# Performance work log

Measured on AMD Instinct MI355X. Metric: run time of the kernel, lower is better.

## Reference

```python
import jax, jax.numpy as jnp
import numpy as np

B, S, E, H = 8, 2048, 512, 4
D = E // H


def setup_inputs() -> dict:
    key = jax.random.key(0)
    ks = jax.random.split(key, 9)
    std = 0.05  # keras 'normal' initializer default stddev
    return {
        "x": jax.random.normal(ks[0], (B, S, E), dtype=jnp.float32),
        "Wq": jax.random.normal(ks[1], (E, E), dtype=jnp.float32) * std,
        "Wk": jax.random.normal(ks[2], (E, E), dtype=jnp.float32) * std,
        "Wv": jax.random.normal(ks[3], (E, E), dtype=jnp.float32) * std,
        "Wepi": jax.random.normal(ks[4], (S, S), dtype=jnp.float32) * std,
        "bq": jax.random.normal(ks[5], (S, 1), dtype=jnp.float32) * std,
        "bk": jax.random.normal(ks[6], (S, 1), dtype=jnp.float32) * std,
        "bv": jax.random.normal(ks[7], (S, 1), dtype=jnp.float32) * std,
        "bo": jax.random.normal(ks[8], (S, 1), dtype=jnp.float32) * std,
    }


def reference(x, Wq, Wk, Wv, Wepi, bq, bk, bv, bo):
    b, s, e = x.shape
    # QKV projections; [S,1] biases broadcast across the feature dim
    q = x @ Wq + bq  # [B,S,E]
    k = x @ Wk + bk
    v = x @ Wv + bv
    # split heads -> [B,H,S,D]
    q = q.reshape(b, s, H, D).transpose(0, 2, 1, 3)
    k = k.reshape(b, s, H, D).transpose(0, 2, 1, 3)
    v = v.reshape(b, s, H, D).transpose(0, 2, 1, 3)
    # NOTE: source scales by sqrt(seq_length), not sqrt(head_dim)
    scale = 1.0 / np.sqrt(float(s)).astype(np.float32)
    scores = jnp.einsum("bhsd,bhtd->bhst", q, k) * scale  # [B,H,S,S]
    attn = jax.nn.softmax(scores, axis=-1)
    # epigenomic multiplicative mask applied AFTER softmax (broadcast [S,S])
    attn = attn * Wepi
    effect = jnp.einsum("bhst,bhtd->bhsd", attn, v)  # [B,H,S,D]
    effect = effect.transpose(0, 2, 1, 3).reshape(b, s, e) + bo
    # original returns attention in merged-batch layout [B*H, S, S]
    return effect, attn.reshape(b * H, s, s)
```

## Files before the change

### kernel.cpp

```cpp
#include <hip/hip_runtime.h>
#include <hip/hip_bf16.h>

constexpr int Bn = 8, Sn = 2048, En = 512, Hn = 4, Dn = 128;
constexpr int BHn = Bn * Hn;
constexpr int Mqkv = Bn * Sn;

typedef __attribute__((ext_vector_type(8))) short short8;
typedef __attribute__((ext_vector_type(4))) float f32x4;

__device__ __forceinline__ unsigned short f2bf(float f) {
  unsigned int u = __builtin_bit_cast(unsigned int, f);
  u += 0x7FFF + ((u >> 16) & 1);
  return (unsigned short)(u >> 16);
}

__device__ __forceinline__ void bar_pub() {
  asm volatile("s_waitcnt lgkmcnt(0)" ::: "memory");
  __builtin_amdgcn_s_barrier();
  asm volatile("" ::: "memory");
}

__global__ __launch_bounds__(256) void qkv_kernel(
    const float* __restrict__ x, const float* __restrict__ Wq,
    const float* __restrict__ Wk, const float* __restrict__ Wv,
    const float* __restrict__ bq, const float* __restrict__ bk,
    const float* __restrict__ bv, unsigned short* __restrict__ qkv) {
  const int z = blockIdx.z;
  const float* W = (z == 0) ? Wq : (z == 1 ? Wk : Wv);
  const float* bias = (z == 0) ? bq : (z == 1 ? bk : bv);
  unsigned short* out = qkv + (size_t)z * BHn * Sn * Dn;

  __shared__ unsigned short As[128][40];
  __shared__ unsigned short BsT[128][40];

  const int t = threadIdx.x;
  const int l = t & 63, w = t >> 6;
  const int wm = w >> 1, wn = w & 1;
  const int m0 = blockIdx.x * 128, n0 = blockIdx.y * 128;

  f32x4 acc[4][4] = {};

  for (int k0 = 0; k0 < En; k0 += 32) {
    __syncthreads();
#pragma unroll
    for (int i = 0; i < 4; ++i) {
      int idx = t + i * 256;
      int row = idx >> 3, c4 = (idx & 7) * 4;
      float4 v = *reinterpret_cast<const float4*>(&x[(size_t)(m0 + row) * En + k0 + c4]);
      ushort4 p;
      p.x = f2bf(v.x); p.y = f2bf(v.y); p.z = f2bf(v.z); p.w = f2bf(v.w);
      *reinterpret_cast<ushort4*>(&As[row][c4]) = p;
    }
#pragma unroll
    for (int i = 0; i < 4; ++i) {
      int idx = t + i * 256;
      int kk = idx >> 5, c4 = (idx & 31) * 4;
      float4 v = *reinterpret_cast<const float4*>(&W[(size_t)(k0 + kk) * En + n0 + c4]);
      BsT[c4 + 0][kk] = f2bf(v.x);
      BsT[c4 + 1][kk] = f2bf(v.y);
      BsT[c4 + 2][kk] = f2bf(v.z);
      BsT[c4 + 3][kk] = f2bf(v.w);
    }
    __syncthreads();

    const int koff = (l >> 4) * 8;
    short8 a[4], bfr[4];
#pragma unroll
    for (int m = 0; m < 4; ++m)
      a[m] = *reinterpret_cast<const short8*>(&As[wm * 64 + m * 16 + (l & 15)][koff]);
#pragma unroll
    for (int n = 0; n < 4; ++n)
      bfr[n] = *reinterpret_cast<const short8*>(&BsT[wn * 64 + n * 16 + (l & 15)][koff]);
#pragma unroll
    for (int m = 0; m < 4; ++m)
#pragma unroll
      for (int n = 0; n < 4; ++n)
        acc[m][n] = __builtin_amdgcn_mfma_f32_16x16x32_bf16(a[m], bfr[n], acc[m][n], 0, 0, 0);
  }

#pragma unroll
  for (int m = 0; m < 4; ++m)
#pragma unroll
    for (int n = 0; n < 4; ++n)
#pragma unroll
      for (int j = 0; j < 4; ++j) {
        int row = m0 + wm * 64 + m * 16 + (l >> 4) * 4 + j;
        int col = n0 + wn * 64 + n * 16 + (l & 15);
        int s = row & (Sn - 1);
        float v = acc[m][n][j] + bias[s];
        int b = row >> 11;
        int h = col >> 7, d = col & 127;
        out[(size_t)((b * Hn + h) * Sn + s) * Dn + d] = f2bf(v);
      }
}

__global__ __launch_bounds__(256) void vtrans_kernel(
    const unsigned short* __restrict__ v, unsigned short* __restrict__ vT) {
  const int s0 = blockIdx.x * 64, d0 = blockIdx.y * 64;
  const int bh = blockIdx.z;
  const unsigned short* vp = v + (size_t)bh * Sn * Dn;
  unsigned short* op = vT + (size_t)bh * Dn * Sn;
  __shared__ unsigned short Ls[64][72];
  const int t = threadIdx.x;
#pragma unroll
  for (int it = 0; it < 2; ++it) {
    int flat = t + it * 256;
    int r = flat >> 3, cc = flat & 7;
    *reinterpret_cast<short8*>(&Ls[r][cc * 8]) =
        *reinterpret_cast<const short8*>(&vp[(size_t)(s0 + r) * Dn + d0 + cc * 8]);
  }
  __syncthreads();
#pragma unroll
  for (int it = 0; it < 2; ++it) {
    int flat = t + it * 256;
    int d = flat >> 3, sc = flat & 7;
    short8 o;
#pragma unroll
    for (int jo = 0; jo < 8; ++jo) {
      int jj = (jo + sc) & 7;
      o[jj] = (short)Ls[sc * 8 + jj][d];
    }
    *reinterpret_cast<short8*>(&op[(size_t)(d0 + d) * Sn + s0 + sc * 8]) = o;
  }
}

__global__ __launch_bounds__(256, 2) void fused_attn4_kernel(
    const unsigned short* __restrict__ qkv, const unsigned short* __restrict__ vT,
    const float* __restrict__ Wepi, const float* __restrict__ bo,
    float* __restrict__ attn, float* __restrict__ effect) {
  const int bh = blockIdx.y;
  const int s0 = blockIdx.x * 64;
  const unsigned short* qp = qkv + (size_t)bh * Sn * Dn;
  const unsigned short* kp = qkv + (size_t)(BHn + bh) * Sn * Dn;
  const unsigned short* vt = vT + (size_t)bh * Dn * Sn;

  __shared__ unsigned short Kb[2][64 * 128];
  __shared__ unsigned short Vt[2][128 * 64];
  __shared__ unsigned short Psw[4][16 * 72];

  const int t = threadIdx.x, l = t & 63, w = t >> 6;
  const int g = l >> 4, i = l & 15;
  const float scale = 0.022097086912079608f;

  short8 aq[4];
#pragma unroll
  for (int ks = 0; ks < 4; ++ks)
    aq[ks] = *reinterpret_cast<const short8*>(
        &qp[(size_t)(s0 + w * 16 + i) * Dn + ks * 32 + g * 8]);

  int ksrc[4], kdst[4], vsrc[4], vdst[4];
#pragma unroll
  for (int it = 0; it < 4; ++it) {
    int flat = t + it * 256;
    int r = flat >> 4, cc = flat & 15;
    ksrc[it] = r * Dn + cc * 8;
    kdst[it] = r * 128 + ((cc ^ (r & 15)) << 3);
    int d = flat >> 3, ct = flat & 7;
    vsrc[it] = d * Sn + ct * 8;
    vdst[it] = d * 64 + ((ct ^ (d & 7)) << 3);
  }

  short8 kreg[4];
#pragma unroll
  for (int it = 0; it < 4; ++it)
    kreg[it] = *reinterpret_cast<const short8*>(&kp[ksrc[it]]);
#pragma unroll
  for (int it = 0; it < 4; ++it)
    *reinterpret_cast<short8*>(&Kb[0][kdst[it]]) = kreg[it];
#pragma unroll
  for (int it = 0; it < 4; ++it)
    kreg[it] = *reinterpret_cast<const short8*>(&kp[(size_t)64 * Dn + ksrc[it]]);
  bar_pub();

  float rs = 0.f;
  for (int kt = 0; kt < 32; ++kt) {
    const int b = kt & 1;
    f32x4 accT[4] = {};
    __builtin_amdgcn_s_setprio(1);
#pragma unroll
    for (int ks = 0; ks < 4; ++ks)
#pragma unroll
      for (int tf = 0; tf < 4; ++tf) {
        short8 ak = *reinterpret_cast<const short8*>(
            &Kb[b][(tf * 16 + i) * 128 + (((ks * 4 + g) ^ i) << 3)]);
        accT[tf] = __builtin_amdgcn_mfma_f32_16x16x32_bf16(ak, aq[ks], accT[tf], 0, 0, 0);
      }
    __builtin_amdgcn_s_setprio(0);
    float p0 = 0.f, p1 = 0.f;
#pragma unroll
    for (int tf = 0; tf < 4; ++tf) {
      p0 += __expf(accT[tf][0] * scale) + __expf(accT[tf][1] * scale);
      p1 += __expf(accT[tf][2] * scale) + __expf(accT[tf][3] * scale);
    }
    rs += p0 + p1;
    if (kt < 31) {
#pragma unroll
      for (int it = 0; it < 4; ++it)
        *reinterpret_cast<short8*>(&Kb[b ^ 1][kdst[it]]) = kreg[it];
      if (kt < 30)
#pragma unroll
        for (int it = 0; it < 4; ++it)
          kreg[it] = *reinterpret_cast<const short8*>(
              &kp[(size_t)(kt + 2) * 64 * Dn + ksrc[it]]);
    }
    bar_pub();
  }
  rs += __shfl_xor(rs, 16);
  rs += __shfl_xor(rs, 32);
  const float rinv = 1.0f / rs;

  short8 vreg[4];
#pragma unroll
  for (int it = 0; it < 4; ++it) {
    kreg[it] = *reinterpret_cast<const short8*>(&kp[ksrc[it]]);
    vreg[it] = *reinterpret_cast<const short8*>(&vt[vsrc[it]]);
  }
#pragma unroll
  for (int it = 0; it < 4; ++it) {
    *reinterpret_cast<short8*>(&Kb[0][kdst[it]]) = kreg[it];
    *reinterpret_cast<short8*>(&Vt[0][vdst[it]]) = vreg[it];
  }
#pragma unroll
  for (int it = 0; it < 4; ++it) {
    kreg[it] = *reinterpret_cast<const short8*>(&kp[(size_t)64 * Dn + ksrc[it]]);
    vreg[it] = *reinterpret_cast<const short8*>(&vt[64 + vsrc[it]]);
  }
  const float* wrow = Wepi + (size_t)(s0 + w * 16 + i) * Sn + g * 4;
  float4 wr[4];
#pragma unroll
  for (int tf = 0; tf < 4; ++tf)
    wr[tf] = *reinterpret_cast<const float4*>(&wrow[tf * 16]);
  bar_pub();

  f32x4 pv[8] = {};
  float* arow = attn + (size_t)bh * Sn * Sn + (size_t)(s0 + w * 16 + i) * Sn;

  for (int kt = 0; kt < 32; ++kt) {
    const int b = kt & 1;
    const int t0 = kt * 64;
    f32x4 accT[4] = {};
    __builtin_amdgcn_s_setprio(1);
#pragma unroll
    for (int ks = 0; ks < 4; ++ks)
#pragma unroll
      for (int tf = 0; tf < 4; ++tf) {
        short8 ak = *reinterpret_cast<const short8*>(
            &Kb[b][(tf * 16 + i) * 128 + (((ks * 4 + g) ^ i) << 3)]);
        accT[tf] = __builtin_amdgcn_mfma_f32_16x16x32_bf16(ak, aq[ks], accT[tf], 0, 0, 0);
      }
    __builtin_amdgcn_s_setprio(0);

    float4 nwr[4];
    if (kt < 31)
#pragma unroll
      for (int tf = 0; tf < 4; ++tf)
        nwr[tf] = *reinterpret_cast<const float4*>(&wrow[t0 + 64 + tf * 16]);

#pragma unroll
    for (int tf = 0; tf < 4; ++tf) {
      float q0 = __expf(accT[tf][0] * scale) * rinv * wr[tf].x;
      float q1 = __expf(accT[tf][1] * scale) * rinv * wr[tf].y;
      float q2 = __expf(accT[tf][2] * scale) * rinv * wr[tf].z;
      float q3 = __expf(accT[tf][3] * scale) * rinv * wr[tf].w;
      float4 pf4 = {q0, q1, q2, q3};
      *reinterpret_cast<float4*>(&arow[t0 + tf * 16 + g * 4]) = pf4;
      ushort4 pk;
      pk.x = f2bf(q0); pk.y = f2bf(q1); pk.z = f2bf(q2); pk.w = f2bf(q3);
      *reinterpret_cast<ushort4*>(&Psw[w][i * 72 + tf * 16 + g * 4]) = pk;
    }

    __builtin_amdgcn_s_setprio(1);
#pragma unroll
    for (int ks2 = 0; ks2 < 2; ++ks2) {
      short8 pa = *reinterpret_cast<const short8*>(&Psw[w][i * 72 + ks2 * 32 + g * 8]);
#pragma unroll
      for (int df = 0; df < 8; ++df) {
        const int d = df * 16 + i;
        short8 bv = *reinterpret_cast<const short8*>(
            &Vt[b][d * 64 + (((ks2 * 4 + g) ^ (d & 7)) << 3)]);
        pv[df] = __builtin_amdgcn_mfma_f32_16x16x32_bf16(pa, bv, pv[df], 0, 0, 0);
      }
    }
    __builtin_amdgcn_s_setprio(0);

    if (kt < 31) {
#pragma unroll
      for (int it = 0; it < 4; ++it) {
        *reinterpret_cast<short8*>(&Kb[b ^ 1][kdst[it]]) = kreg[it];
        *reinterpret_cast<short8*>(&Vt[b ^ 1][vdst[it]]) = vreg[it];
      }
      if (kt < 30)
#pragma unroll
        for (int it = 0; it < 4; ++it) {
          kreg[it] = *reinterpret_cast<const short8*>(
              &kp[(size_t)(t0 + 128) * Dn + ksrc[it]]);
          vreg[it] = *reinterpret_cast<const short8*>(&vt[t0 + 128 + vsrc[it]]);
        }
#pragma unroll
      for (int tf = 0; tf < 4; ++tf) wr[tf] = nwr[tf];
    }
    bar_pub();
  }

  const int b_ = bh >> 2, h_ = bh & 3;
#pragma unroll
  for (int j = 0; j < 4; ++j) {
    const int row = s0 + w * 16 + g * 4 + j;
    const float bias = bo[row];
#pragma unroll
    for (int df = 0; df < 8; ++df)
      effect[(size_t)(b_ * Sn + row) * En + h_ * Dn + df * 16 + i] = pv[df][j] + bias;
  }
}

extern "C" void kernel_launch(void* const* d_in, const int* in_sizes, int n_in,
                              void* d_out, int out_size, void* d_ws, size_t ws_size,
                              hipStream_t stream) {
  const float* x    = (const float*)d_in[0];
  const float* Wq   = (const float*)d_in[1];
  const float* Wk   = (const float*)d_in[2];
  const float* Wv   = (const float*)d_in[3];
  const float* Wepi = (const float*)d_in[4];
  const float* bq   = (const float*)d_in[5];
  const float* bk   = (const float*)d_in[6];
  const float* bv   = (const float*)d_in[7];
  const float* bo   = (const float*)d_in[8];

  float* effect = (float*)d_out;
  float* attn = effect + (size_t)Bn * Sn * En;
  unsigned short* qkv = (unsigned short*)d_ws;
  unsigned short* vT = qkv + (size_t)3 * BHn * Sn * Dn;

  qkv_kernel<<<dim3(Mqkv / 128, En / 128, 3), 256, 0, stream>>>(x, Wq, Wk, Wv, bq, bk, bv, qkv);
  vtrans_kernel<<<dim3(Sn / 64, Dn / 64, BHn), 256, 0, stream>>>(
      qkv + (size_t)2 * BHn * Sn * Dn, vT);
  fused_attn4_kernel<<<dim3(Sn / 64, BHn), 256, 0, stream>>>(qkv, vT, Wepi, bo, attn, effect);
}
```

Baseline: 411.1 us.

## Repartition attention warps over key columns and head-dim, software-pipeline PV by one tile

Each wave now holds all 64 query rows in registers and computes scores for its own 16-key slice, so every K fragment loaded from LDS is reused across four MFMAs instead of one. The PV product is split across waves by head-dim slice, with P shared through a double-buffered, swizzled LDS tile and its MFMAs delayed by one iteration so they overlap the next tile's QK^T. Row sums for the softmax are reduced across waves through LDS. This cuts LDS traffic for K and V fragments, but it raises register pressure (16 Q fragments held per wave) and adds a cross-wave reduction plus extra LDS for P.

```diff
diff --git a/kernel.cpp b/kernel.cpp
--- a/kernel.cpp
+++ b/kernel.cpp
@@ -124,7 +124,7 @@
   }
 }
 
-__global__ __launch_bounds__(256, 2) void fused_attn4_kernel(
+__global__ __launch_bounds__(256, 2) void fused_attn5_kernel(
     const unsigned short* __restrict__ qkv, const unsigned short* __restrict__ vT,
     const float* __restrict__ Wepi, const float* __restrict__ bo,
     float* __restrict__ attn, float* __restrict__ effect) {
@@ -136,17 +136,19 @@
 
   __shared__ unsigned short Kb[2][64 * 128];
   __shared__ unsigned short Vt[2][128 * 64];
-  __shared__ unsigned short Psw[4][16 * 72];
+  __shared__ unsigned short Ps[2][64 * 64];
 
   const int t = threadIdx.x, l = t & 63, w = t >> 6;
   const int g = l >> 4, i = l & 15;
   const float scale = 0.022097086912079608f;
 
-  short8 aq[4];
-#pragma unroll
-  for (int ks = 0; ks < 4; ++ks)
-    aq[ks] = *reinterpret_cast<const short8*>(
-        &qp[(size_t)(s0 + w * 16 + i) * Dn + ks * 32 + g * 8]);
+  short8 aq[4][4];
+#pragma unroll
+  for (int sf = 0; sf < 4; ++sf)
+#pragma unroll
+    for (int ks = 0; ks < 4; ++ks)
+      aq[sf][ks] = *reinterpret_cast<const short8*>(
+          &qp[(size_t)(s0 + sf * 16 + i) * Dn + ks * 32 + g * 8]);
 
   int ksrc[4], kdst[4], vsrc[4], vdst[4];
 #pragma unroll
@@ -172,27 +174,24 @@
     kreg[it] = *reinterpret_cast<const short8*>(&kp[(size_t)64 * Dn + ksrc[it]]);
   bar_pub();
 
-  float rs = 0.f;
+  float rs[4] = {0.f, 0.f, 0.f, 0.f};
   for (int kt = 0; kt < 32; ++kt) {
     const int b = kt & 1;
     f32x4 accT[4] = {};
     __builtin_amdgcn_s_setprio(1);
 #pragma unroll
-    for (int ks = 0; ks < 4; ++ks)
-#pragma unroll
-      for (int tf = 0; tf < 4; ++tf) {
-        short8 ak = *reinterpret_cast<const short8*>(
-            &Kb[b][(tf * 16 + i) * 128 + (((ks * 4 + g) ^ i) << 3)]);
-        accT[tf] = __builtin_amdgcn_mfma_f32_16x16x32_bf16(ak, aq[ks], accT[tf], 0, 0, 0);
-      }
+    for (int ks = 0; ks < 4; ++ks) {
+      short8 ak = *reinterpret_cast<const short8*>(
+          &Kb[b][(w * 16 + i) * 128 + (((ks * 4 + g) ^ i) << 3)]);
+#pragma unroll
+      for (int sf = 0; sf < 4; ++sf)
+        accT[sf] = __builtin_amdgcn_mfma_f32_16x16x32_bf16(ak, aq[sf][ks], accT[sf], 0, 0, 0);
+    }
     __builtin_amdgcn_s_setprio(0);
-    float p0 = 0.f, p1 = 0.f;
-#pragma unroll
-    for (int tf = 0; tf < 4; ++tf) {
-      p0 += __expf(accT[tf][0] * scale) + __expf(accT[tf][1] * scale);
-      p1 += __expf(accT[tf][2] * scale) + __expf(accT[tf][3] * scale);
-    }
-    rs += p0 + p1;
+#pragma unroll
+    for (int sf = 0; sf < 4; ++sf)
+      rs[sf] += __expf(accT[sf][0] * scale) + __expf(accT[sf][1] * scale) +
+                __expf(accT[sf][2] * scale) + __expf(accT[sf][3] * scale);
     if (kt < 31) {
 #pragma unroll
       for (int it = 0; it < 4; ++it)
@@ -205,112 +204,149 @@
     }
     bar_pub();
   }
-  rs += __shfl_xor(rs, 16);
-  rs += __shfl_xor(rs, 32);
-  const float rinv = 1.0f / rs;
+
+  float* wpart = reinterpret_cast<float*>(&Ps[0][0]);
+#pragma unroll
+  for (int sf = 0; sf < 4; ++sf) {
+    float v = rs[sf];
+    v += __shfl_xor(v, 16);
+    v += __shfl_xor(v, 32);
+    if (l < 16) wpart[w * 64 + sf * 16 + l] = v;
+  }
+  bar_pub();
+  float rinv[4];
+#pragma unroll
+  for (int sf = 0; sf < 4; ++sf) {
+    const int s = sf * 16 + i;
+    rinv[sf] = 1.0f / (wpart[s] + wpart[64 + s] + wpart[128 + s] + wpart[192 + s]);
+  }
 
   short8 vreg[4];
 #pragma unroll
-  for (int it = 0; it < 4; ++it) {
+  for (int it = 0; it < 4; ++it)
     kreg[it] = *reinterpret_cast<const short8*>(&kp[ksrc[it]]);
-    vreg[it] = *reinterpret_cast<const short8*>(&vt[vsrc[it]]);
-  }
-#pragma unroll
-  for (int it = 0; it < 4; ++it) {
+#pragma unroll
+  for (int it = 0; it < 4; ++it)
     *reinterpret_cast<short8*>(&Kb[0][kdst[it]]) = kreg[it];
-    *reinterpret_cast<short8*>(&Vt[0][vdst[it]]) = vreg[it];
-  }
 #pragma unroll
   for (int it = 0; it < 4; ++it) {
     kreg[it] = *reinterpret_cast<const short8*>(&kp[(size_t)64 * Dn + ksrc[it]]);
-    vreg[it] = *reinterpret_cast<const short8*>(&vt[64 + vsrc[it]]);
-  }
-  const float* wrow = Wepi + (size_t)(s0 + w * 16 + i) * Sn + g * 4;
+    vreg[it] = *reinterpret_cast<const short8*>(&vt[vsrc[it]]);
+  }
+  const float* wbase = Wepi + (size_t)(s0 + i) * Sn + w * 16 + g * 4;
+  float* abase = attn + (size_t)bh * Sn * Sn + (size_t)(s0 + i) * Sn + w * 16 + g * 4;
   float4 wr[4];
 #pragma unroll
-  for (int tf = 0; tf < 4; ++tf)
-    wr[tf] = *reinterpret_cast<const float4*>(&wrow[tf * 16]);
+  for (int sf = 0; sf < 4; ++sf)
+    wr[sf] = *reinterpret_cast<const float4*>(&wbase[(size_t)sf * 16 * Sn]);
   bar_pub();
 
-  f32x4 pv[8] = {};
-  float* arow = attn + (size_t)bh * Sn * Sn + (size_t)(s0 + w * 16 + i) * Sn;
-
+  f32x4 pv[4][2] = {};
   for (int kt = 0; kt < 32; ++kt) {
     const int b = kt & 1;
     const int t0 = kt * 64;
     f32x4 accT[4] = {};
     __builtin_amdgcn_s_setprio(1);
 #pragma unroll
-    for (int ks = 0; ks < 4; ++ks)
-#pragma unroll
-      for (int tf = 0; tf < 4; ++tf) {
-        short8 ak = *reinterpret_cast<const short8*>(
-            &Kb[b][(tf * 16 + i) * 128 + (((ks * 4 + g) ^ i) << 3)]);
-        accT[tf] = __builtin_amdgcn_mfma_f32_16x16x32_bf16(ak, aq[ks], accT[tf], 0, 0, 0);
+    for (int ks = 0; ks < 4; ++ks) {
+      short8 ak = *reinterpret_cast<const short8*>(
+          &Kb[b][(w * 16 + i) * 128 + (((ks * 4 + g) ^ i) << 3)]);
+#pragma unroll
+      for (int sf = 0; sf < 4; ++sf)
+        accT[sf] = __builtin_amdgcn_mfma_f32_16x16x32_bf16(ak, aq[sf][ks], accT[sf], 0, 0, 0);
+    }
+    if (kt > 0) {
+#pragma unroll
+      for (int ks2 = 0; ks2 < 2; ++ks2) {
+        short8 pa[4];
+#pragma unroll
+        for (int sf = 0; sf < 4; ++sf)
+          pa[sf] = *reinterpret_cast<const short8*>(
+              &Ps[b ^ 1][(sf * 16 + i) * 64 + (((ks2 * 4 + g) ^ (i & 7)) << 3)]);
+#pragma unroll
+        for (int nf = 0; nf < 2; ++nf) {
+          const int d = w * 32 + nf * 16 + i;
+          short8 bv = *reinterpret_cast<const short8*>(
+              &Vt[b ^ 1][d * 64 + (((ks2 * 4 + g) ^ (i & 7)) << 3)]);
+#pragma unroll
+          for (int sf = 0; sf < 4; ++sf)
+            pv[sf][nf] =
+                __builtin_amdgcn_mfma_f32_16x16x32_bf16(pa[sf], bv, pv[sf][nf], 0, 0, 0);
+        }
       }
+    }
     __builtin_amdgcn_s_setprio(0);
 
-    float4 nwr[4];
-    if (kt < 31)
-#pragma unroll
-      for (int tf = 0; tf < 4; ++tf)
-        nwr[tf] = *reinterpret_cast<const float4*>(&wrow[t0 + 64 + tf * 16]);
-
-#pragma unroll
-    for (int tf = 0; tf < 4; ++tf) {
-      float q0 = __expf(accT[tf][0] * scale) * rinv * wr[tf].x;
-      float q1 = __expf(accT[tf][1] * scale) * rinv * wr[tf].y;
-      float q2 = __expf(accT[tf][2] * scale) * rinv * wr[tf].z;
-      float q3 = __expf(accT[tf][3] * scale) * rinv * wr[tf].w;
+#pragma unroll
+    for (int sf = 0; sf < 4; ++sf) {
+      float q0 = __expf(accT[sf][0] * scale) * rinv[sf] * wr[sf].x;
+      float q1 = __expf(accT[sf][1] * scale) * rinv[sf] * wr[sf].y;
+      float q2 = __expf(accT[sf][2] * scale) * rinv[sf] * wr[sf].z;
+      float q3 = __expf(accT[sf][3] * scale) * rinv[sf] * wr[sf].w;
       float4 pf4 = {q0, q1, q2, q3};
-      *reinterpret_cast<float4*>(&arow[t0 + tf * 16 + g * 4]) = pf4;
+      *reinterpret_cast<float4*>(&abase[(size_t)sf * 16 * Sn + t0]) = pf4;
       ushort4 pk;
       pk.x = f2bf(q0); pk.y = f2bf(q1); pk.z = f2bf(q2); pk.w = f2bf(q3);
-      *reinterpret_cast<ushort4*>(&Psw[w][i * 72 + tf * 16 + g * 4]) = pk;
-    }
-
-    __builtin_amdgcn_s_setprio(1);
-#pragma unroll
-    for (int ks2 = 0; ks2 < 2; ++ks2) {
-      short8 pa = *reinterpret_cast<const short8*>(&Psw[w][i * 72 + ks2 * 32 + g * 8]);
-#pragma unroll
-      for (int df = 0; df < 8; ++df) {
-        const int d = df * 16 + i;
-        short8 bv = *reinterpret_cast<const short8*>(
-            &Vt[b][d * 64 + (((ks2 * 4 + g) ^ (d & 7)) << 3)]);
-        pv[df] = __builtin_amdgcn_mfma_f32_16x16x32_bf16(pa, bv, pv[df], 0, 0, 0);
-      }
-    }
-    __builtin_amdgcn_s_setprio(0);
-
-    if (kt < 31) {
-#pragma unroll
-      for (int it = 0; it < 4; ++it) {
+      const int row = sf * 16 + i;
+      *reinterpret_cast<ushort4*>(
+          &Ps[b][row * 64 + (((w * 2 + (g >> 1)) ^ (i & 7)) << 3) + (g & 1) * 4]) = pk;
+    }
+    if (kt < 31)
+#pragma unroll
+      for (int sf = 0; sf < 4; ++sf)
+        wr[sf] = *reinterpret_cast<const float4*>(&wbase[(size_t)sf * 16 * Sn + t0 + 64]);
+
+    if (kt < 31)
+#pragma unroll
+      for (int it = 0; it < 4; ++it)
         *reinterpret_cast<short8*>(&Kb[b ^ 1][kdst[it]]) = kreg[it];
-        *reinterpret_cast<short8*>(&Vt[b ^ 1][vdst[it]]) = vreg[it];
-      }
-      if (kt < 30)
-#pragma unroll
-        for (int it = 0; it < 4; ++it) {
-          kreg[it] = *reinterpret_cast<const short8*>(
-              &kp[(size_t)(t0 + 128) * Dn + ksrc[it]]);
-          vreg[it] = *reinterpret_cast<const short8*>(&vt[t0 + 128 + vsrc[it]]);
-        }
-#pragma unroll
-      for (int tf = 0; tf < 4; ++tf) wr[tf] = nwr[tf];
-    }
+#pragma unroll
+    for (int it = 0; it < 4; ++it)
+      *reinterpret_cast<short8*>(&Vt[b][vdst[it]]) = vreg[it];
+    if (kt < 30)
+#pragma unroll
+      for (int it = 0; it < 4; ++it)
+        kreg[it] = *reinterpret_cast<const short8*>(
+            &kp[(size_t)(kt + 2) * 64 * Dn + ksrc[it]]);
+    if (kt < 31)
+#pragma unroll
+      for (int it = 0; it < 4; ++it)
+        vreg[it] = *reinterpret_cast<const short8*>(&vt[t0 + 64 + vsrc[it]]);
     bar_pub();
   }
 
+  __builtin_amdgcn_s_setprio(1);
+#pragma unroll
+  for (int ks2 = 0; ks2 < 2; ++ks2) {
+    short8 pa[4];
+#pragma unroll
+    for (int sf = 0; sf < 4; ++sf)
+      pa[sf] = *reinterpret_cast<const short8*>(
+          &Ps[1][(sf * 16 + i) * 64 + (((ks2 * 4 + g) ^ (i & 7)) << 3)]);
+#pragma unroll
+    for (int nf = 0; nf < 2; ++nf) {
+      const int d = w * 32 + nf * 16 + i;
+      short8 bv = *reinterpret_cast<const short8*>(
+          &Vt[1][d * 64 + (((ks2 * 4 + g) ^ (i & 7)) << 3)]);
+#pragma unroll
+      for (int sf = 0; sf < 4; ++sf)
+        pv[sf][nf] = __builtin_amdgcn_mfma_f32_16x16x32_bf16(pa[sf], bv, pv[sf][nf], 0, 0, 0);
+    }
+  }
+  __builtin_amdgcn_s_setprio(0);
+
   const int b_ = bh >> 2, h_ = bh & 3;
 #pragma unroll
-  for (int j = 0; j < 4; ++j) {
-    const int row = s0 + w * 16 + g * 4 + j;
-    const float bias = bo[row];
-#pragma unroll
-    for (int df = 0; df < 8; ++df)
-      effect[(size_t)(b_ * Sn + row) * En + h_ * Dn + df * 16 + i] = pv[df][j] + bias;
-  }
+  for (int sf = 0; sf < 4; ++sf)
+#pragma unroll
+    for (int j = 0; j < 4; ++j) {
+      const int row = s0 + sf * 16 + g * 4 + j;
+      const float bias = bo[row];
+#pragma unroll
+      for (int nf = 0; nf < 2; ++nf)
+        effect[(size_t)(b_ * Sn + row) * En + h_ * Dn + w * 32 + nf * 16 + i] =
+            pv[sf][nf][j] + bias;
+    }
 }
 
 extern "C" void kernel_launch(void* const* d_in, const int* in_sizes, int n_in,
@@ -334,5 +370,5 @@
   qkv_kernel<<<dim3(Mqkv / 128, En / 128, 3), 256, 0, stream>>>(x, Wq, Wk, Wv, bq, bk, bv, qkv);
   vtrans_kernel<<<dim3(Sn / 64, Dn / 64, BHn), 256, 0, stream>>>(
       qkv + (size_t)2 * BHn * Sn * Dn, vT);
-  fused_attn4_kernel<<<dim3(Sn / 64, BHn), 256, 0, stream>>>(qkv, vT, Wepi, bo, attn, effect);
-}
+  fused_attn5_kernel<<<dim3(Sn / 64, BHn), 256, 0, stream>>>(qkv, vT, Wepi, bo, attn, effect);
+}
```

After: 406.5 us. No clear change (-1.1%).
